# Optimization experiments

Measured on AMD Instinct MI355X. Metric: run time of the kernel, lower is better.

Reference implementation:

```python
import jax, jax.numpy as jnp
import numpy as np

B, T, D = 2, 2048, 1024   # batch, seq, d_model
E, K, H = 8, 2, 704       # routed experts, topk, expert hidden
SH = 704 * 2              # shared-expert hidden = moe_hidden * num_shared_experts
EPS = 1e-20               # topk_norm_epsilon
STD = 0.02                # init_weight_std


def setup_inputs() -> dict:
    key = jax.random.key(0)
    ks = jax.random.split(key, 8)
    return {
        "x":   jax.random.normal(ks[0], (B, T, D), jnp.float32),
        "Wg":  jax.random.normal(ks[1], (E, D), jnp.float32) * STD,   # router experts_weights
        "W1":  jax.random.normal(ks[2], (E, D, H), jnp.float32) * STD,  # gate proj per expert
        "W3":  jax.random.normal(ks[3], (E, D, H), jnp.float32) * STD,  # up proj per expert
        "W2":  jax.random.normal(ks[4], (E, H, D), jnp.float32) * STD,  # down proj per expert
        "Ws1": jax.random.normal(ks[5], (D, SH), jnp.float32) * STD,    # shared expert
        "Ws3": jax.random.normal(ks[6], (D, SH), jnp.float32) * STD,
        "Ws2": jax.random.normal(ks[7], (SH, D), jnp.float32) * STD,
    }


def reference(x, Wg, W1, W3, W2, Ws1, Ws3, Ws2):
    b, t, d = x.shape
    n = b * t
    xf = x.reshape(n, d)
    # softmax gating + topk + scatter back into dense [N,E] gate matrix
    gates = jax.nn.softmax(xf @ Wg.T, axis=-1)                      # [N,E]
    top_v, top_i = jax.lax.top_k(gates, K)                          # [N,K]
    masked = jnp.zeros_like(gates).at[jnp.arange(n)[:, None], top_i].set(top_v)
    masked = masked / (masked.sum(-1, keepdims=True) + EPS)         # normalized_moe_gates
    # per-expert SwiGLU FFN over all tokens, then gate-weighted combine
    h = jnp.einsum('nd,edh->enh', xf, W1)                           # [E,N,H]
    g = jnp.einsum('nd,edh->enh', xf, W3)
    y = jnp.einsum('enh,ehd->end', jax.nn.silu(h) * g, W2)          # [E,N,D]
    routed = jnp.einsum('ne,end->nd', masked, y)                    # combine
    shared = (jax.nn.silu(xf @ Ws1) * (xf @ Ws3)) @ Ws2             # shared experts
    return (routed + shared).reshape(b, t, d)
```

## Files before the change

### kernel.cpp

```cpp
#include <hip/hip_runtime.h>
#include <math.h>

typedef __bf16 bf16;
typedef __attribute__((ext_vector_type(8))) __bf16 bf16x8;
typedef __attribute__((ext_vector_type(4))) __bf16 bf16x4;
typedef __attribute__((ext_vector_type(4))) float f32x4;

#define NTOK 4096
#define DM   1024
#define NE   8
#define NEX  10
#define HE   704

#define OFF_CNT   0u
#define OFF_TOK   256u
#define OFF_WGT   131328u
#define OFF_XB    262400u
#define OFF_W1T   8651008u
#define OFF_W3T   20185344u
#define OFF_W2T   31719680u
#define OFF_WS1T  43254016u
#define OFF_WS3T  46137600u
#define OFF_WS2T  49021184u
#define OFF_ACT   51904768u
#define OFF_EIDS  74973440u
#define OFF_MAP1  OFF_EIDS
#define OFF_MAP2  (OFF_EIDS + 2048u)
#define OFF_GW    74989824u
#define OFF_SLOT  75022592u
#define OFF_YR    OFF_W1T

__device__ __forceinline__ void async_cp16(const bf16* g, bf16* l)
{
    __builtin_amdgcn_global_load_lds(
        (const __attribute__((address_space(1))) unsigned int*)g,
        (__attribute__((address_space(3))) unsigned int*)l, 16, 0, 0);
}

__global__ void cvt_x_kernel(const float* __restrict__ x, bf16* __restrict__ xb, int n4)
{
    int i = blockIdx.x * blockDim.x + threadIdx.x;
    if (i >= n4) return;
    float4 v = ((const float4*)x)[i];
    bf16x4 o;
    o[0] = (bf16)v.x; o[1] = (bf16)v.y; o[2] = (bf16)v.z; o[3] = (bf16)v.w;
    ((bf16x4*)xb)[i] = o;
}

__global__ __launch_bounds__(256) void transpose_all(
    const float* __restrict__ W1, const float* __restrict__ W3, const float* __restrict__ W2,
    const float* __restrict__ Ws1, const float* __restrict__ Ws3, const float* __restrict__ Ws2,
    bf16* __restrict__ w1t, bf16* __restrict__ w3t, bf16* __restrict__ w2t,
    bf16* __restrict__ ws1t, bf16* __restrict__ ws3t, bf16* __restrict__ ws2t)
{
    int id = blockIdx.x;
    const float* src; bf16* dst; int C, rt, ct, nkt;
    if (id < 5632)       { int t = id;         int e = t / 704, m = t % 704; C = 704;
                           src = W1 + (size_t)e * 1024 * 704;  dst = w1t + (size_t)e * 720896;
                           ct = m % 22; rt = m / 22; nkt = 32; }
    else if (id < 11264) { int t = id - 5632;  int e = t / 704, m = t % 704; C = 704;
                           src = W3 + (size_t)e * 1024 * 704;  dst = w3t + (size_t)e * 720896;
                           ct = m % 22; rt = m / 22; nkt = 32; }
    else if (id < 16896) { int t = id - 11264; int e = t / 704, m = t % 704; C = 1024;
                           src = W2 + (size_t)e * 704 * 1024;  dst = w2t + (size_t)e * 720896;
                           ct = m % 32; rt = m / 32; nkt = 22; }
    else if (id < 18304) { int t = id - 16896; C = 1408; src = Ws1;
                           ct = t % 44; rt = t / 44; nkt = 32;
                           int ep = (ct >= 22) ? 1 : 0; ct -= 22 * ep;
                           src += (size_t)704 * ep;
                           dst = ws1t + (size_t)ep * 720896; }
    else if (id < 19712) { int t = id - 18304; C = 1408; src = Ws3;
                           ct = t % 44; rt = t / 44; nkt = 32;
                           int ep = (ct >= 22) ? 1 : 0; ct -= 22 * ep;
                           src += (size_t)704 * ep;
                           dst = ws3t + (size_t)ep * 720896; }
    else                 { int t = id - 19712; C = 1024; src = Ws2;
                           ct = t % 32; rt = t / 32; nkt = 22;
                           int ep = (rt >= 22) ? 1 : 0; rt -= 22 * ep;
                           src += (size_t)704 * 1024 * ep;
                           dst = ws2t + (size_t)ep * 720896; }

    __shared__ float tl[32][33];
    int c0 = ct * 32, r0 = rt * 32;
    int row  = threadIdx.x >> 3;
    int col4 = (threadIdx.x & 7) * 4;
    float4 v = *(const float4*)&src[(size_t)(r0 + row) * C + c0 + col4];
    tl[row][col4 + 0] = v.x; tl[row][col4 + 1] = v.y;
    tl[row][col4 + 2] = v.z; tl[row][col4 + 3] = v.w;
    __syncthreads();
    int n  = c0 + row;
    int ng = n >> 4, nr = n & 15;
    int kt = rt;
    int cc = col4 >> 3, j = col4 & 7;
    bf16x4 o;
    o[0] = (bf16)tl[col4 + 0][row];
    o[1] = (bf16)tl[col4 + 1][row];
    o[2] = (bf16)tl[col4 + 2][row];
    o[3] = (bf16)tl[col4 + 3][row];
    *(bf16x4*)&dst[(size_t)(((ng * nkt + kt) << 9) + (((cc << 4) | nr) << 3) + j)] = o;
}

__global__ __launch_bounds__(256) void router_logits(
    const float* __restrict__ x, const float* __restrict__ Wg,
    int* __restrict__ eids, float2* __restrict__ gw)
{
    int n    = blockIdx.x * 4 + (threadIdx.x >> 6);
    int lane = threadIdx.x & 63;
    const float* xrow = x + (size_t)n * DM;
    float xr[16];
    #pragma unroll
    for (int j = 0; j < 16; j++) xr[j] = xrow[lane + 64 * j];
    float logit[NE];
    #pragma unroll
    for (int e = 0; e < NE; e++) {
        const float* wr = Wg + e * DM;
        float s = 0.f;
        #pragma unroll
        for (int j = 0; j < 16; j++) s += xr[j] * wr[lane + 64 * j];
        #pragma unroll
        for (int off = 32; off; off >>= 1) s += __shfl_xor(s, off, 64);
        logit[e] = s;
    }
    if (lane == 0) {
        int i0 = 0;
        #pragma unroll
        for (int e = 1; e < NE; e++) if (logit[e] > logit[i0]) i0 = e;
        int i1 = (i0 == 0) ? 1 : 0;
        #pragma unroll
        for (int e = 0; e < NE; e++) if (e != i0 && logit[e] > logit[i1]) i1 = e;
        float m = logit[0];
        #pragma unroll
        for (int e = 1; e < NE; e++) m = fmaxf(m, logit[e]);
        float denom = 0.f;
        #pragma unroll
        for (int e = 0; e < NE; e++) denom += expf(logit[e] - m);
        float g0 = expf(logit[i0] - m) / denom;
        float g1 = expf(logit[i1] - m) / denom;
        float inv = 1.f / (g0 + g1 + 1e-20f);
        eids[n] = i0 | (i1 << 16);
        gw[n] = make_float2(g0 * inv, g1 * inv);
    }
}

__global__ __launch_bounds__(128) void build_lists(
    const int* __restrict__ eids, const float2* __restrict__ gw,
    int* __restrict__ cnt, int* __restrict__ tok, float* __restrict__ wgt,
    int2* __restrict__ slots)
{
    __shared__ int lcnt[NE];
    __shared__ int gbase[NE];
    int t = threadIdx.x;
    int n = blockIdx.x * 128 + t;
    if (t < NE) lcnt[t] = 0;
    __syncthreads();
    int packed = eids[n];
    float2 w = gw[n];
    int e0 = packed & 0xffff, e1 = packed >> 16;
    int s0 = atomicAdd(&lcnt[e0], 1);
    int s1 = atomicAdd(&lcnt[e1], 1);
    __syncthreads();
    if (t < NE) gbase[t] = atomicAdd(&cnt[t], lcnt[t]);
    __syncthreads();
    int p0 = gbase[e0] + s0, p1 = gbase[e1] + s1;
    tok[e0 * NTOK + p0] = n; wgt[e0 * NTOK + p0] = w.x;
    tok[e1 * NTOK + p1] = n; wgt[e1 * NTOK + p1] = w.y;
    slots[n] = make_int2((e0 << 16) | p0, (e1 << 16) | p1);
}

__global__ void prefix_kernel(const int* __restrict__ cnt, int* __restrict__ pfx,
                              int* __restrict__ map1, int* __restrict__ map2)
{
    if (threadIdx.x != 0) return;
    int s = 0;
    for (int e = 0; e < NEX; e++) { pfx[e] = s; s += (e < NE) ? cnt[e] : NTOK; }
    pfx[NEX] = s;
    int n1 = 0;
    for (int e = 0; e < NEX; e++) {
        int c = (e < NE) ? cnt[e] : NTOK;
        int ntl = (c + 127) >> 7;
        for (int t = 0; t < ntl; t++) map1[n1++] = (e << 16) | t;
    }
    pfx[11] = n1;
    int n2 = 0;
    for (int e = 0; e < NE; e++) {
        int c = cnt[e];
        int ntl = (c + 127) >> 7;
        for (int t = 0; t < ntl; t++) map2[n2++] = (e << 16) | t;
    }
    for (int t = 0; t < NTOK / 128; t++) map2[n2++] = (NE << 16) | t;
    pfx[12] = n2;
}


__global__ __launch_bounds__(256) void gemm1_swiglu(
    const bf16* __restrict__ xb,
    const bf16* __restrict__ w1t, const bf16* __restrict__ w3t,
    const bf16* __restrict__ ws1t, const bf16* __restrict__ ws3t,
    bf16* __restrict__ act,
    const int* __restrict__ cnt, const int* __restrict__ pfx,
    const int* __restrict__ tok, const int* __restrict__ map)
{
    if ((int)blockIdx.y >= pfx[11]) return;
    int ent = map[blockIdx.y];
    int e  = ent >> 16;
    int m0 = (ent & 0xffff) << 7;
    int count = (e < NE) ? cnt[e] : NTOK;
    int h0 = blockIdx.x * 64;
    int base = pfx[e];
    const bf16 *B1, *B3;
    if (e < NE) { B1 = w1t + (size_t)e * 720896;         B3 = w3t + (size_t)e * 720896; }
    else        { B1 = ws1t + (size_t)(e - NE) * 720896; B3 = ws3t + (size_t)(e - NE) * 720896; }
    const int* tlist = (e < NE) ? tok + e * NTOK : nullptr;

    __shared__ bf16 As[2][8 * 512];
    __shared__ bf16 B1s[2][4 * 512];
    __shared__ bf16 B3s[2][4 * 512];

    int tid = threadIdx.x, w = tid >> 6, lane = tid & 63;

    int r3 = lane >> 2;
    int cx = (lane & 3) ^ ((r3 >> 1) & 3);
    int sA0 = m0 + 32 * w + r3, sA1 = sA0 + 16;
    int rA0 = tlist ? (sA0 < count ? tlist[sA0] : 0) : (sA0 < count ? sA0 : 0);
    int rA1 = tlist ? (sA1 < count ? tlist[sA1] : 0) : (sA1 < count ? sA1 : 0);
    const bf16* ga0 = xb + (size_t)rA0 * DM + cx * 8;
    const bf16* ga1 = xb + (size_t)rA1 * DM + cx * 8;
    const bf16* gb1 = B1 + ((size_t)((h0 >> 4) + w) * 32) * 512 + lane * 8;
    const bf16* gb3 = B3 + ((size_t)((h0 >> 4) + w) * 32) * 512 + lane * 8;
    bf16* aA0 = &As[0][0]  + (2 * w) * 512;
    bf16* aA1 = aA0 + 512;
    bf16* aB1 = &B1s[0][0] + w * 512;
    bf16* aB3 = &B3s[0][0] + w * 512;

    int rl = lane & 15, ch = lane >> 4;
    int uA = 4 * rl + (ch ^ ((rl >> 1) & 3));
    int gA = (w & 1) * 4;
    int gB = (w >> 1) * 2;
    int wm = (w & 1) * 64, wn = (w >> 1) * 32;

    f32x4 acch[4][2], accg[4][2];
    #pragma unroll
    for (int i = 0; i < 4; i++)
        #pragma unroll
        for (int j = 0; j < 2; j++) {
            acch[i][j] = (f32x4){0.f, 0.f, 0.f, 0.f};
            accg[i][j] = (f32x4){0.f, 0.f, 0.f, 0.f};
        }

#define STAGE1(buf) do { \
        async_cp16(ga0, aA0 + (buf) * 4096); \
        async_cp16(ga1, aA1 + (buf) * 4096); \
        async_cp16(gb1, aB1 + (buf) * 2048); \
        async_cp16(gb3, aB3 + (buf) * 2048); \
        ga0 += 32; ga1 += 32; gb1 += 512; gb3 += 512; \
    } while (0)

    STAGE1(0);
    __syncthreads();
    for (int k0 = 0; k0 < 32; k0++) {
        int cur = k0 & 1;
        if (k0 < 31) STAGE1(cur ^ 1);
        const bf16* Ab  = &As[0][0]  + cur * 4096;
        const bf16* B1b = &B1s[0][0] + cur * 2048;
        const bf16* B3b = &B3s[0][0] + cur * 2048;
        bf16x8 af[4], b1f[2], b3f[2];
        #pragma unroll
        for (int i = 0; i < 4; i++) af[i] = *(const bf16x8*)(Ab + (gA + i) * 512 + uA * 8);
        #pragma unroll
        for (int j = 0; j < 2; j++) {
            b1f[j] = *(const bf16x8*)(B1b + (gB + j) * 512 + lane * 8);
            b3f[j] = *(const bf16x8*)(B3b + (gB + j) * 512 + lane * 8);
        }
        #pragma unroll
        for (int i = 0; i < 4; i++)
            #pragma unroll
            for (int j = 0; j < 2; j++) {
                acch[i][j] = __builtin_amdgcn_mfma_f32_16x16x32_bf16(af[i], b1f[j], acch[i][j], 0, 0, 0);
                accg[i][j] = __builtin_amdgcn_mfma_f32_16x16x32_bf16(af[i], b3f[j], accg[i][j], 0, 0, 0);
            }
        __syncthreads();
    }
#undef STAGE1

    #pragma unroll
    for (int i = 0; i < 4; i++)
        #pragma unroll
        for (int j = 0; j < 2; j++)
            #pragma unroll
            for (int r = 0; r < 4; r++) {
                int row = wm + i * 16 + ch * 4 + r;
                int s2 = m0 + row;
                if (s2 < count) {
                    float hv = acch[i][j][r], gv = accg[i][j][r];
                    float a = hv / (1.f + expf(-hv)) * gv;
                    act[(size_t)(base + s2) * HE + h0 + wn + j * 16 + rl] = (bf16)a;
                }
            }
}

__global__ __launch_bounds__(256) void gemm2_all(
    const bf16* __restrict__ act,
    const bf16* __restrict__ w2t, const bf16* __restrict__ ws2t,
    bf16* __restrict__ yr, float* __restrict__ out,
    const int* __restrict__ cnt, const int* __restrict__ pfx,
    const float* __restrict__ wgt, const int* __restrict__ map)
{
    if ((int)blockIdx.y >= pfx[12]) return;
    int ent = map[blockIdx.y];
    int e  = ent >> 16;
    int m0 = (ent & 0xffff) << 7;
    int d0 = blockIdx.x * 128;

    __shared__ bf16 As[2][8 * 512];
    __shared__ bf16 Bs[2][8 * 512];

    int tid = threadIdx.x, w = tid >> 6, lane = tid & 63;

    int r3 = lane >> 2;
    int cx = (lane & 3) ^ ((r3 >> 1) & 3);
    int sA0 = m0 + 32 * w + r3, sA1 = sA0 + 16;
    int rl = lane & 15, ch = lane >> 4;
    int uA = 4 * rl + (ch ^ ((rl >> 1) & 3));
    int gA = (w & 1) * 4, gB = (w >> 1) * 4;
    int wm = (w & 1) * 64, wn = (w >> 1) * 64;

    bf16* aA0 = &As[0][0] + (2 * w) * 512;
    bf16* aA1 = aA0 + 512;
    bf16* aB0 = &Bs[0][0] + (2 * w) * 512;
    bf16* aB1 = aB0 + 512;

    int count, base; const bf16* Bp;
    if (e < NE) { count = cnt[e]; base = pfx[e]; Bp = w2t + (size_t)e * 720896; }
    else        { count = NTOK;   base = NTOK * 2; Bp = ws2t; }

    int a0 = (sA0 < count) ? (base + sA0) : base;
    int a1 = (sA1 < count) ? (base + sA1) : base;
    const bf16* ga0 = act + (size_t)a0 * HE + cx * 8;
    const bf16* ga1 = act + (size_t)a1 * HE + cx * 8;
    const bf16* gb0 = Bp + ((size_t)((d0 >> 4) + 2 * w) * 22) * 512 + lane * 8;
    const bf16* gb1 = Bp + ((size_t)((d0 >> 4) + 2 * w + 1) * 22) * 512 + lane * 8;

    f32x4 acc[4][4];
    #pragma unroll
    for (int i = 0; i < 4; i++)
        #pragma unroll
        for (int j = 0; j < 4; j++) acc[i][j] = (f32x4){0.f, 0.f, 0.f, 0.f};

#define STAGE2(buf) do { \
        async_cp16(ga0, aA0 + (buf) * 4096); \
        async_cp16(ga1, aA1 + (buf) * 4096); \
        async_cp16(gb0, aB0 + (buf) * 4096); \
        async_cp16(gb1, aB1 + (buf) * 4096); \
        ga0 += 32; ga1 += 32; gb0 += 512; gb1 += 512; \
    } while (0)

    int total = (e < NE) ? 22 : 44;
    STAGE2(0);
    int ns = 1;
    __syncthreads();
    for (int kt = 0; kt < total; kt++) {
        int cur = kt & 1;
        if (ns < total) {
            if (ns == 22) {
                ga0 = act + (size_t)(12288 + sA0) * HE + cx * 8;
                ga1 = act + (size_t)(12288 + sA1) * HE + cx * 8;
                const bf16* B2 = ws2t + 720896;
                gb0 = B2 + ((size_t)((d0 >> 4) + 2 * w) * 22) * 512 + lane * 8;
                gb1 = B2 + ((size_t)((d0 >> 4) + 2 * w + 1) * 22) * 512 + lane * 8;
            }
            STAGE2(cur ^ 1);
            ns++;
        }
        const bf16* Ab = &As[0][0] + cur * 4096;
        const bf16* Bb = &Bs[0][0] + cur * 4096;
        bf16x8 af[4], bf_[4];
        #pragma unroll
        for (int i = 0; i < 4; i++) af[i]  = *(const bf16x8*)(Ab + (gA + i) * 512 + uA * 8);
        #pragma unroll
        for (int j = 0; j < 4; j++) bf_[j] = *(const bf16x8*)(Bb + (gB + j) * 512 + lane * 8);
        #pragma unroll
        for (int i = 0; i < 4; i++)
            #pragma unroll
            for (int j = 0; j < 4; j++)
                acc[i][j] = __builtin_amdgcn_mfma_f32_16x16x32_bf16(af[i], bf_[j], acc[i][j], 0, 0, 0);
        __syncthreads();
    }
#undef STAGE2

    if (e < NE) {
        const float* wl = wgt + e * NTOK;
        #pragma unroll
        for (int i = 0; i < 4; i++) {
            #pragma unroll
            for (int r = 0; r < 4; r++) {
                int row = wm + i * 16 + ch * 4 + r;
                int s2 = m0 + row;
                if (s2 < count) {
                    float wt = wl[s2];
                    bf16* yrow = yr + (size_t)(base + s2) * DM + d0 + wn;
                    #pragma unroll
                    for (int j = 0; j < 4; j++)
                        yrow[j * 16 + rl] = (bf16)(wt * acc[i][j][r]);
                }
            }
        }
    } else {
        #pragma unroll
        for (int i = 0; i < 4; i++) {
            #pragma unroll
            for (int r = 0; r < 4; r++) {
                int row = wm + i * 16 + ch * 4 + r;
                float* orow = out + (size_t)(m0 + row) * DM + d0 + wn;
                #pragma unroll
                for (int j = 0; j < 4; j++)
                    orow[j * 16 + rl] = acc[i][j][r];
            }
        }
    }
}

__global__ __launch_bounds__(256) void fuse_add(
    const bf16* __restrict__ yr, const int2* __restrict__ slots,
    const int* __restrict__ pfx, float* __restrict__ out)
{
    int n = blockIdx.x;
    int2 s = slots[n];
    int slot0 = pfx[s.x >> 16] + (s.x & 0xffff);
    int slot1 = pfx[s.y >> 16] + (s.y & 0xffff);
    const bf16* y0 = yr + (size_t)slot0 * DM;
    const bf16* y1 = yr + (size_t)slot1 * DM;
    float* orow = out + (size_t)n * DM;
    int d = threadIdx.x * 4;
    bf16x4 a = *(const bf16x4*)(y0 + d);
    bf16x4 b = *(const bf16x4*)(y1 + d);
    float4 o = *(float4*)(orow + d);
    o.x += (float)a[0] + (float)b[0];
    o.y += (float)a[1] + (float)b[1];
    o.z += (float)a[2] + (float)b[2];
    o.w += (float)a[3] + (float)b[3];
    *(float4*)(orow + d) = o;
}

extern "C" void kernel_launch(void* const* d_in, const int* in_sizes, int n_in,
                              void* d_out, int out_size, void* d_ws, size_t ws_size,
                              hipStream_t stream)
{
    const float* x   = (const float*)d_in[0];
    const float* Wg  = (const float*)d_in[1];
    const float* W1  = (const float*)d_in[2];
    const float* W3  = (const float*)d_in[3];
    const float* W2  = (const float*)d_in[4];
    const float* Ws1 = (const float*)d_in[5];
    const float* Ws3 = (const float*)d_in[6];
    const float* Ws2 = (const float*)d_in[7];
    float* out = (float*)d_out;
    char*  ws  = (char*)d_ws;

    int*    cnt   = (int*)(ws + OFF_CNT);
    int*    pfx   = (int*)(ws + OFF_CNT + 32);
    int*    tok   = (int*)(ws + OFF_TOK);
    float*  wgt   = (float*)(ws + OFF_WGT);
    bf16*   xb    = (bf16*)(ws + OFF_XB);
    bf16*   w1t   = (bf16*)(ws + OFF_W1T);
    bf16*   w3t   = (bf16*)(ws + OFF_W3T);
    bf16*   w2t   = (bf16*)(ws + OFF_W2T);
    bf16*   ws1t  = (bf16*)(ws + OFF_WS1T);
    bf16*   ws3t  = (bf16*)(ws + OFF_WS3T);
    bf16*   ws2t  = (bf16*)(ws + OFF_WS2T);
    bf16*   act   = (bf16*)(ws + OFF_ACT);
    int*    eids  = (int*)(ws + OFF_EIDS);
    int*    map1  = (int*)(ws + OFF_MAP1);
    int*    map2  = (int*)(ws + OFF_MAP2);
    float2* gw    = (float2*)(ws + OFF_GW);
    int2*   slots = (int2*)(ws + OFF_SLOT);
    bf16*   yr    = (bf16*)(ws + OFF_YR);

    hipMemsetAsync(ws, 0, 256, stream);

    cvt_x_kernel<<<4096, 256, 0, stream>>>(x, xb, NTOK * DM / 4);
    transpose_all<<<21120, 256, 0, stream>>>(W1, W3, W2, Ws1, Ws3, Ws2,
                                             w1t, w3t, w2t, ws1t, ws3t, ws2t);
    router_logits<<<1024, 256, 0, stream>>>(x, Wg, eids, gw);
    build_lists<<<32, 128, 0, stream>>>(eids, gw, cnt, tok, wgt, slots);
    prefix_kernel<<<1, 64, 0, stream>>>(cnt, pfx, map1, map2);

    gemm1_swiglu<<<dim3(HE / 64, 136, 1), 256, 0, stream>>>(
        xb, w1t, w3t, ws1t, ws3t, act, cnt, pfx, tok, map1);

    gemm2_all<<<dim3(DM / 128, 104, 1), 256, 0, stream>>>(
        act, w2t, ws2t, yr, out, cnt, pfx, wgt, map2);

    fuse_add<<<NTOK, 256, 0, stream>>>(yr, slots, pfx, out);
}
```

Baseline: 312.7 us.

## Schedule expert GEMM tiles per XCD for L2 locality with balanced maps

Rebuilds the gemm1 and gemm2 tile maps so that all tiles of one expert land on the same XCD, using blockIdx modulo 8 as the XCD slot. Tiles are balanced greedily across the eight slots, and unused slots are padded with -1 for early exit. The goal is to keep each expert's weights in a single XCD's L2 rather than spreading them across all of them. The trade-offs are a serial single-thread map build, possible load imbalance, and launching empty blocks.

```diff
diff --git a/kernel.cpp b/kernel.cpp
--- a/kernel.cpp
+++ b/kernel.cpp
@@ -11,6 +11,9 @@
 #define NE   8
 #define NEX  10
 #define HE   704
+
+#define MAP1_CAP 224
+#define MAP2_CAP 128
 
 #define OFF_CNT   0u
 #define OFF_TOK   256u
@@ -25,7 +28,7 @@
 #define OFF_ACT   51904768u
 #define OFF_EIDS  74973440u
 #define OFF_MAP1  OFF_EIDS
-#define OFF_MAP2  (OFF_EIDS + 2048u)
+#define OFF_MAP2  (OFF_EIDS + 8192u)
 #define OFF_GW    74989824u
 #define OFF_SLOT  75022592u
 #define OFF_YR    OFF_W1T
@@ -170,27 +173,62 @@
 __global__ void prefix_kernel(const int* __restrict__ cnt, int* __restrict__ pfx,
                               int* __restrict__ map1, int* __restrict__ map2)
 {
-    if (threadIdx.x != 0) return;
+    int t = threadIdx.x;
+    for (int i = t; i < 8 * MAP1_CAP; i += 64) map1[i] = -1;
+    for (int i = t; i < 8 * MAP2_CAP; i += 64) map2[i] = -1;
+    __syncthreads();
+    if (t != 0) return;
     int s = 0;
     for (int e = 0; e < NEX; e++) { pfx[e] = s; s += (e < NE) ? cnt[e] : NTOK; }
     pfx[NEX] = s;
-    int n1 = 0;
+
+    int ntl[NEX];
+    int tot1 = 0;
     for (int e = 0; e < NEX; e++) {
         int c = (e < NE) ? cnt[e] : NTOK;
-        int ntl = (c + 127) >> 7;
-        for (int t = 0; t < ntl; t++) map1[n1++] = (e << 16) | t;
-    }
-    pfx[11] = n1;
-    int n2 = 0;
-    for (int e = 0; e < NE; e++) {
-        int c = cnt[e];
-        int ntl = (c + 127) >> 7;
-        for (int t = 0; t < ntl; t++) map2[n2++] = (e << 16) | t;
-    }
-    for (int t = 0; t < NTOK / 128; t++) map2[n2++] = (NE << 16) | t;
-    pfx[12] = n2;
-}
-
+        ntl[e] = (c + 127) >> 7;
+        tot1 += ntl[e];
+    }
+    {
+        int len[8] = {0,0,0,0,0,0,0,0};
+        int avg = (tot1 * 11 + 7) >> 3;
+        int k = 0;
+        for (int e = 0; e < NEX; e++) {
+            k = 0;
+            for (int q = 1; q < 8; q++) if (len[q] < len[k]) k = q;
+            for (int tt = 0; tt < ntl[e]; tt++) {
+                if (len[k] >= avg) {
+                    k = 0;
+                    for (int q = 1; q < 8; q++) if (len[q] < len[k]) k = q;
+                }
+                for (int h = 0; h < 11; h++)
+                    map1[(len[k] + h) * 8 + k] = (e << 20) | (tt << 8) | h;
+                len[k] += 11;
+            }
+        }
+    }
+    {
+        int len[8] = {0,0,0,0,0,0,0,0};
+        int tot2 = 0;
+        for (int e = 0; e <= NE; e++) tot2 += (e < NE) ? ntl[e] : (NTOK >> 7);
+        int avg = tot2;
+        int k = 0;
+        for (int e = 0; e <= NE; e++) {
+            int nt2 = (e < NE) ? ntl[e] : (NTOK >> 7);
+            k = 0;
+            for (int q = 1; q < 8; q++) if (len[q] < len[k]) k = q;
+            for (int tt = 0; tt < nt2; tt++) {
+                if (len[k] >= avg) {
+                    k = 0;
+                    for (int q = 1; q < 8; q++) if (len[q] < len[k]) k = q;
+                }
+                for (int d = 0; d < 8; d++)
+                    map2[(len[k] + d) * 8 + k] = (e << 20) | (tt << 8) | d;
+                len[k] += 8;
+            }
+        }
+    }
+}
 
 __global__ __launch_bounds__(256) void gemm1_swiglu(
     const bf16* __restrict__ xb,
@@ -200,12 +238,13 @@
     const int* __restrict__ cnt, const int* __restrict__ pfx,
     const int* __restrict__ tok, const int* __restrict__ map)
 {
-    if ((int)blockIdx.y >= pfx[11]) return;
-    int ent = map[blockIdx.y];
-    int e  = ent >> 16;
-    int m0 = (ent & 0xffff) << 7;
+    int b = blockIdx.x;
+    int ent = map[(b >> 3) * 8 + (b & 7)];
+    if (ent < 0) return;
+    int e  = ent >> 20;
+    int m0 = ((ent >> 8) & 0xfff) << 7;
+    int h0 = (ent & 255) * 64;
     int count = (e < NE) ? cnt[e] : NTOK;
-    int h0 = blockIdx.x * 64;
     int base = pfx[e];
     const bf16 *B1, *B3;
     if (e < NE) { B1 = w1t + (size_t)e * 720896;         B3 = w3t + (size_t)e * 720896; }
@@ -305,11 +344,12 @@
     const int* __restrict__ cnt, const int* __restrict__ pfx,
     const float* __restrict__ wgt, const int* __restrict__ map)
 {
-    if ((int)blockIdx.y >= pfx[12]) return;
-    int ent = map[blockIdx.y];
-    int e  = ent >> 16;
-    int m0 = (ent & 0xffff) << 7;
-    int d0 = blockIdx.x * 128;
+    int b = blockIdx.x;
+    int ent = map[(b >> 3) * 8 + (b & 7)];
+    if (ent < 0) return;
+    int e  = ent >> 20;
+    int m0 = ((ent >> 8) & 0xfff) << 7;
+    int d0 = (ent & 255) * 128;
 
     __shared__ bf16 As[2][8 * 512];
     __shared__ bf16 Bs[2][8 * 512];
@@ -484,10 +524,10 @@
     build_lists<<<32, 128, 0, stream>>>(eids, gw, cnt, tok, wgt, slots);
     prefix_kernel<<<1, 64, 0, stream>>>(cnt, pfx, map1, map2);
 
-    gemm1_swiglu<<<dim3(HE / 64, 136, 1), 256, 0, stream>>>(
+    gemm1_swiglu<<<8 * MAP1_CAP, 256, 0, stream>>>(
         xb, w1t, w3t, ws1t, ws3t, act, cnt, pfx, tok, map1);
 
-    gemm2_all<<<dim3(DM / 128, 104, 1), 256, 0, stream>>>(
+    gemm2_all<<<8 * MAP2_CAP, 256, 0, stream>>>(
         act, w2t, ws2t, yr, out, cnt, pfx, wgt, map2);
 
     fuse_add<<<NTOK, 256, 0, stream>>>(yr, slots, pfx, out);
```

Result: slower. 357.2 us (+14.2%).
